# Optimization experiments

Measured on AMD Instinct MI355X. Metric: run time of the kernel, lower is better.

## Reference

```python
import jax, jax.numpy as jnp
import numpy as np

B, N, C, H = 8, 1024, 768, 12
D = C // H          # head_dim = 64
M = 2 * D           # rand_feat_dim = 128
SCALE = D ** -0.5
EPS = 1e-12         # F.normalize eps


def _feature_map(z, rand_matrix):
    # z: [B,H,N,D] already multiplied by sqrt(scale); proj: [H,D,M]
    logits = jnp.einsum('bhnd,hdm->bhnm', z, rand_matrix)
    sqnorm = 0.5 * jnp.sum(z * z, axis=-1, keepdims=True)
    return jnp.exp(logits - sqnorm) * (M ** -0.5)


def setup_inputs() -> dict:
    key = jax.random.key(0)
    k1, k2, k3, k4, k5 = jax.random.split(key, 5)
    x = jax.random.normal(k1, (B, N, C), dtype=jnp.float32)
    qkv_w = jax.random.normal(k2, (3 * C, C), dtype=jnp.float32) * 0.02
    proj_w = jax.random.normal(k3, (C, C), dtype=jnp.float32) * 0.02
    proj_b = jax.random.normal(k4, (C,), dtype=jnp.float32) * 0.02
    rand_matrix = jax.random.normal(k5, (H, D, M), dtype=jnp.float32)
    return {"x": x, "qkv_w": qkv_w, "proj_w": proj_w, "proj_b": proj_b,
            "rand_matrix": rand_matrix}


def reference(x, qkv_w, proj_w, proj_b, rand_matrix):
    b, n, c = x.shape
    # qkv projection (torch Linear, no bias): [B,N,3C] -> [3,B,H,N,D]
    qkv = (x @ qkv_w.T).reshape(b, n, 3, H, D).transpose(2, 0, 3, 1, 4)
    q, k, v = qkv[0], qkv[1], qkv[2]
    sq = SCALE ** 0.5
    qf = _feature_map(q * sq, rand_matrix)   # [B,H,N,M]
    kf = _feature_map(k * sq, rand_matrix)   # [B,H,N,M]
    attn = jnp.einsum('bhnm,bhkm->bhnk', qf, kf)          # explicit O(N^2)
    denom = jnp.maximum(jnp.sum(jnp.abs(attn), axis=-1, keepdims=True), EPS)
    attn = attn / denom                                   # L1 normalize
    out = jnp.einsum('bhnk,bhkd->bhnd', attn, v)          # [B,H,N,D]
    out = out.transpose(0, 2, 1, 3).reshape(b, n, c)
    return out @ proj_w.T + proj_b
```

## Files before the change

kernel.cpp:

```cpp
#include <hip/hip_runtime.h>
#include <hip/hip_bf16.h>

#define PB 8
#define PN 1024
#define PC 768
#define PH 12
#define PD 64
#define PM 128
#define SQ 0.35355339059327373f
#define MSCALE 0.08838834764831843f

typedef _Float16 f16;
typedef f16 f16x8 __attribute__((ext_vector_type(8)));
typedef f16 f16x4 __attribute__((ext_vector_type(4)));
typedef float f32x4 __attribute__((ext_vector_type(4)));

#define GLL(src, dst) __builtin_amdgcn_global_load_lds( \
    (const __attribute__((address_space(1))) void*)(src), \
    (__attribute__((address_space(3))) void*)(dst), 16, 0, 0)

__global__ __launch_bounds__(192) void conv_all(
        const float* __restrict__ x, const float* __restrict__ qkv_w,
        const float* __restrict__ proj_w, const float* __restrict__ rm,
        f16* __restrict__ Ax, f16* __restrict__ Bqk, f16* __restrict__ Bp,
        f16* __restrict__ Rt, float* __restrict__ kvf, float* __restrict__ sf)
{
    const int bid = blockIdx.x;
    const int t = threadIdx.x;
    if (bid < 11264) {
        const float* src; f16* dst; int r;
        if (bid < 8192)       { src = x;      dst = Ax;  r = bid; }
        else if (bid < 10496) { src = qkv_w;  dst = Bqk; r = bid - 8192; }
        else                  { src = proj_w; dst = Bp;  r = bid - 10496; }
        const int c = t * 4;
        float4 v = *(const float4*)&src[(size_t)r * PC + c];
        f16x4 hv;
        hv.x = (f16)v.x; hv.y = (f16)v.y; hv.z = (f16)v.z; hv.w = (f16)v.w;
        *(f16x4*)&dst[(size_t)r * PC + c] = hv;
    } else if (bid < 11276) {
        const int h = bid - 11264;
        for (int e = t; e < PD * PM; e += 192)
            Rt[(size_t)h * 8192 + e] = (f16)rm[(size_t)h * 8192 + (e & 63) * PM + (e >> 6)];
    } else if (bid < 12300) {
        float4 z = make_float4(0.f, 0.f, 0.f, 0.f);
        *(float4*)&kvf[(size_t)(bid - 11276) * 768 + t * 4] = z;
    } else {
        float4 z = make_float4(0.f, 0.f, 0.f, 0.f);
        *(float4*)&sf[(size_t)(bid - 12300) * 768 + t * 4] = z;
    }
}

__global__ __launch_bounds__(256) void gemm_qkv(
        const f16* __restrict__ A,
        const f16* __restrict__ Bm,
        f16* __restrict__ zq, f16* __restrict__ zk, f16* __restrict__ vh,
        float* __restrict__ sqq, float* __restrict__ sqk)
{
    __shared__ f16 As[128 * 64];
    __shared__ f16 Bs[128 * 64];
    const int t = threadIdx.x;
    const int wave = t >> 6, lane = t & 63;
    const int wm = wave >> 1, wn = wave & 1;
    const int bi = blockIdx.x * 128, bj = blockIdx.y * 128;

    f32x4 acc[4][4] = {};

    const int rowi = lane >> 3;
    const int cb = (lane & 7) ^ ((lane >> 4) & 3);
    const f16* ApE = A + (size_t)(bi + wave * 32 + rowi) * PC + cb * 8;
    const f16* ApO = A + (size_t)(bi + wave * 32 + rowi) * PC + (cb ^ 4) * 8;
    const f16* BpE = Bm + (size_t)(bj + wave * 32 + rowi) * PC + cb * 8;
    const f16* BpO = Bm + (size_t)(bj + wave * 32 + rowi) * PC + (cb ^ 4) * 8;
    f16* AsB = &As[wave * 32 * 64];
    f16* BsB = &Bs[wave * 32 * 64];

    const int q4 = lane >> 4;
    for (int kt = 0; kt < 12; ++kt) {
        const int k0 = kt * 64;
        __syncthreads();
        GLL(ApE + k0,               AsB);
        GLL(ApO + k0 + (size_t) 8 * PC, AsB + 8 * 64);
        GLL(ApE + k0 + (size_t)16 * PC, AsB + 16 * 64);
        GLL(ApO + k0 + (size_t)24 * PC, AsB + 24 * 64);
        GLL(BpE + k0,               BsB);
        GLL(BpO + k0 + (size_t) 8 * PC, BsB + 8 * 64);
        GLL(BpE + k0 + (size_t)16 * PC, BsB + 16 * 64);
        GLL(BpO + k0 + (size_t)24 * PC, BsB + 24 * 64);
        __syncthreads();

        #pragma unroll
        for (int kh = 0; kh < 2; ++kh) {
            f16x8 af[4], bf[4];
            #pragma unroll
            for (int i = 0; i < 4; ++i) {
                const int r = wm * 64 + i * 16 + (lane & 15);
                const int p = (kh * 4 + q4) ^ ((r >> 1) & 7);
                af[i] = *(const f16x8*)&As[r * 64 + p * 8];
            }
            #pragma unroll
            for (int j = 0; j < 4; ++j) {
                const int r = wn * 64 + j * 16 + (lane & 15);
                const int p = (kh * 4 + q4) ^ ((r >> 1) & 7);
                bf[j] = *(const f16x8*)&Bs[r * 64 + p * 8];
            }
            #pragma unroll
            for (int i = 0; i < 4; ++i)
                #pragma unroll
                for (int j = 0; j < 4; ++j)
                    acc[i][j] = __builtin_amdgcn_mfma_f32_16x16x32_f16(af[i], bf[j], acc[i][j], 0, 0, 0);
        }
    }

    const int quad = lane >> 4, cc = lane & 15;
    const int colbase = bj + wn * 64;
    const int b = bi >> 10;
    if (colbase < 1536) {
        const int which = colbase >= 768;
        const int h = (colbase - which * 768) >> 6;
        f16* zdst = which ? zk : zq;
        float* sdst = which ? sqk : sqq;
        const size_t bh = (size_t)(b * PH + h);
        #pragma unroll
        for (int i = 0; i < 4; ++i) {
            const int row0 = bi + wm * 64 + i * 16 + quad * 4;
            #pragma unroll
            for (int r = 0; r < 4; ++r) {
                const int n = (row0 + r) & 1023;
                f16 zh[4]; float psq = 0.f;
                #pragma unroll
                for (int j = 0; j < 4; ++j) {
                    zh[j] = (f16)(acc[i][j][r] * SQ);
                    float zf = (float)zh[j];
                    psq += zf * zf;
                }
                psq += __shfl_xor(psq, 1, 64);
                psq += __shfl_xor(psq, 2, 64);
                psq += __shfl_xor(psq, 4, 64);
                psq += __shfl_xor(psq, 8, 64);
                if (cc == 0) sdst[(bh << 10) + n] = 0.5f * psq;
                f16* zp = zdst + (((bh << 10) + n) << 6);
                #pragma unroll
                for (int j = 0; j < 4; ++j) zp[j * 16 + cc] = zh[j];
            }
        }
    } else {
        const int h = (colbase - 1536) >> 6;
        const size_t bh = (size_t)(b * PH + h);
        #pragma unroll
        for (int i = 0; i < 4; ++i) {
            const int row0 = bi + wm * 64 + i * 16 + quad * 4;
            #pragma unroll
            for (int r = 0; r < 4; ++r) {
                const int n = (row0 + r) & 1023;
                f16* vp = vh + (((bh << 10) + n) << 6);
                #pragma unroll
                for (int j = 0; j < 4; ++j) vp[j * 16 + cc] = (f16)acc[i][j][r];
            }
        }
    }
}

__global__ __launch_bounds__(256) void feat_kv(
        const f16* __restrict__ zk, const f16* __restrict__ Rt,
        const float* __restrict__ sqk, const f16* __restrict__ vh,
        float* __restrict__ kvf, float* __restrict__ sf)
{
    __shared__ __align__(16) char smem[52224];
    f16* As = (f16*)smem;
    f16* Bs = (f16*)(smem + 16384);
    f16* Pt = (f16*)smem;
    f16* vT = (f16*)(smem + 34816);
    __shared__ float sqs[128];

    const int t = threadIdx.x;
    const int wave = t >> 6, lane = t & 63;
    const int wm = wave >> 1, wn = wave & 1;
    const int nt = blockIdx.x, bh = blockIdx.y;
    const int h = bh % PH;

    const f16* A = zk + (((size_t)bh << 10) + nt * 128) * 64;
    const f16* Bm = Rt + (size_t)h * (PM * PD);

    if (t < 128) sqs[t] = sqk[((size_t)bh << 10) + nt * 128 + t];

    const int rowi = lane >> 3;
    const int cb = (lane & 7) ^ ((lane >> 4) & 3);
    const f16* ApE = A + (size_t)(wave * 32 + rowi) * 64 + cb * 8;
    const f16* ApO = A + (size_t)(wave * 32 + rowi) * 64 + (cb ^ 4) * 8;
    const f16* BpE = Bm + (size_t)(wave * 32 + rowi) * 64 + cb * 8;
    const f16* BpO = Bm + (size_t)(wave * 32 + rowi) * 64 + (cb ^ 4) * 8;
    f16* AsB = &As[wave * 32 * 64];
    f16* BsB = &Bs[wave * 32 * 64];
    GLL(ApE,            AsB);
    GLL(ApO + 8 * 64,   AsB + 8 * 64);
    GLL(ApE + 16 * 64,  AsB + 16 * 64);
    GLL(ApO + 24 * 64,  AsB + 24 * 64);
    GLL(BpE,            BsB);
    GLL(BpO + 8 * 64,   BsB + 8 * 64);
    GLL(BpE + 16 * 64,  BsB + 16 * 64);
    GLL(BpO + 24 * 64,  BsB + 24 * 64);
    __syncthreads();

    const int q4 = lane >> 4;
    f32x4 acc[4][4] = {};
    #pragma unroll
    for (int kh = 0; kh < 2; ++kh) {
        f16x8 af[4], bf[4];
        #pragma unroll
        for (int i = 0; i < 4; ++i) {
            const int r = wm * 64 + i * 16 + (lane & 15);
            const int p = (kh * 4 + q4) ^ ((r >> 1) & 7);
            af[i] = *(const f16x8*)&As[r * 64 + p * 8];
        }
        #pragma unroll
        for (int j = 0; j < 4; ++j) {
            const int r = wn * 64 + j * 16 + (lane & 15);
            const int p = (kh * 4 + q4) ^ ((r >> 1) & 7);
            bf[j] = *(const f16x8*)&Bs[r * 64 + p * 8];
        }
        #pragma unroll
        for (int i = 0; i < 4; ++i)
            #pragma unroll
            for (int j = 0; j < 4; ++j)
                acc[i][j] = __builtin_amdgcn_mfma_f32_16x16x32_f16(af[i], bf[j], acc[i][j], 0, 0, 0);
    }

    const int quad = lane >> 4, cc = lane & 15;
    __syncthreads();

    #pragma unroll
    for (int i = 0; i < 4; ++i) {
        #pragma unroll
        for (int j = 0; j < 4; ++j) {
            const int col = wn * 64 + j * 16 + cc;
            #pragma unroll
            for (int r = 0; r < 4; ++r) {
                const int rl = wm * 64 + i * 16 + quad * 4 + r;
                Pt[col * 136 + rl] = (f16)(__expf(acc[i][j][r] - sqs[rl]) * MSCALE);
            }
        }
    }
    {
        const int vn = t >> 1;
        const int vhf = (t & 1) * 32;
        const f16* vbase = vh + (((size_t)bh << 10) + nt * 128 + vn) * 64 + vhf;
        #pragma unroll
        for (int k = 0; k < 4; ++k) {
            f16x8 vv = *(const f16x8*)&vbase[k * 8];
            #pragma unroll
            for (int e = 0; e < 8; ++e)
                vT[(vhf + k * 8 + e) * 136 + vn] = vv[e];
        }
    }
    __syncthreads();

    f32x4 acc2[4][2] = {};
    #pragma unroll
    for (int kt = 0; kt < 4; ++kt) {
        const int kb = kt * 32 + (lane >> 4) * 8;
        f16x8 af2[4], bf2[2];
        #pragma unroll
        for (int i = 0; i < 4; ++i)
            af2[i] = *(const f16x8*)&Pt[(wm * 64 + i * 16 + (lane & 15)) * 136 + kb];
        #pragma unroll
        for (int j = 0; j < 2; ++j)
            bf2[j] = *(const f16x8*)&vT[(wn * 32 + j * 16 + (lane & 15)) * 136 + kb];
        #pragma unroll
        for (int i = 0; i < 4; ++i)
            #pragma unroll
            for (int j = 0; j < 2; ++j)
                acc2[i][j] = __builtin_amdgcn_mfma_f32_16x16x32_f16(af2[i], bf2[j], acc2[i][j], 0, 0, 0);
    }

    float* kvo = kvf + (size_t)bh * 8192;
    #pragma unroll
    for (int i = 0; i < 4; ++i) {
        #pragma unroll
        for (int j = 0; j < 2; ++j) {
            const int d = wn * 32 + j * 16 + cc;
            #pragma unroll
            for (int r = 0; r < 4; ++r) {
                const int m = wm * 64 + i * 16 + quad * 4 + r;
                atomicAdd(&kvo[m * 64 + d], acc2[i][j][r]);
            }
        }
    }
    {
        const int sm = t >> 1, shf = (t & 1) * 64;
        float sp = 0.f;
        #pragma unroll
        for (int k = 0; k < 8; ++k) {
            f16x8 pv = *(const f16x8*)&Pt[sm * 136 + shf + k * 8];
            #pragma unroll
            for (int e = 0; e < 8; ++e) sp += (float)pv[e];
        }
        sp += __shfl_xor(sp, 1, 64);
        if ((t & 1) == 0) atomicAdd(&sf[(size_t)bh * 128 + sm], sp);
    }
}

__global__ __launch_bounds__(256) void feat_apply(
        const f16* __restrict__ zq, const f16* __restrict__ Rt,
        const float* __restrict__ sqq, const float* __restrict__ kvf,
        const float* __restrict__ sf, f16* __restrict__ ohA)
{
    __shared__ __align__(16) char smem[52224];
    f16* As = (f16*)smem;
    f16* Bs = (f16*)(smem + 16384);
    f16* Pn = (f16*)smem;
    f16* kvT = (f16*)(smem + 34816);
    __shared__ float sqs[128], ssm[128], dns[128];

    const int t = threadIdx.x;
    const int wave = t >> 6, lane = t & 63;
    const int wm = wave >> 1, wn = wave & 1;
    const int nt = blockIdx.x, bh = blockIdx.y;
    const int b = bh / PH, h = bh % PH;

    const f16* A = zq + (((size_t)bh << 10) + nt * 128) * 64;
    const f16* Bm = Rt + (size_t)h * (PM * PD);

    if (t < 128) {
        sqs[t] = sqq[((size_t)bh << 10) + nt * 128 + t];
        ssm[t] = sf[(size_t)bh * 128 + t];
    }

    const int rowi = lane >> 3;
    const int cb = (lane & 7) ^ ((lane >> 4) & 3);
    const f16* ApE = A + (size_t)(wave * 32 + rowi) * 64 + cb * 8;
    const f16* ApO = A + (size_t)(wave * 32 + rowi) * 64 + (cb ^ 4) * 8;
    const f16* BpE = Bm + (size_t)(wave * 32 + rowi) * 64 + cb * 8;
    const f16* BpO = Bm + (size_t)(wave * 32 + rowi) * 64 + (cb ^ 4) * 8;
    f16* AsB = &As[wave * 32 * 64];
    f16* BsB = &Bs[wave * 32 * 64];
    GLL(ApE,            AsB);
    GLL(ApO + 8 * 64,   AsB + 8 * 64);
    GLL(ApE + 16 * 64,  AsB + 16 * 64);
    GLL(ApO + 24 * 64,  AsB + 24 * 64);
    GLL(BpE,            BsB);
    GLL(BpO + 8 * 64,   BsB + 8 * 64);
    GLL(BpE + 16 * 64,  BsB + 16 * 64);
    GLL(BpO + 24 * 64,  BsB + 24 * 64);
    __syncthreads();

    const int q4 = lane >> 4;
    f32x4 acc[4][4] = {};
    #pragma unroll
    for (int kh = 0; kh < 2; ++kh) {
        f16x8 af[4], bf[4];
        #pragma unroll
        for (int i = 0; i < 4; ++i) {
            const int r = wm * 64 + i * 16 + (lane & 15);
            const int p = (kh * 4 + q4) ^ ((r >> 1) & 7);
            af[i] = *(const f16x8*)&As[r * 64 + p * 8];
        }
        #pragma unroll
        for (int j = 0; j < 4; ++j) {
            const int r = wn * 64 + j * 16 + (lane & 15);
            const int p = (kh * 4 + q4) ^ ((r >> 1) & 7);
            bf[j] = *(const f16x8*)&Bs[r * 64 + p * 8];
        }
        #pragma unroll
        for (int i = 0; i < 4; ++i)
            #pragma unroll
            for (int j = 0; j < 4; ++j)
                acc[i][j] = __builtin_amdgcn_mfma_f32_16x16x32_f16(af[i], bf[j], acc[i][j], 0, 0, 0);
    }

    const int quad = lane >> 4, cc = lane & 15;
    __syncthreads();

    #pragma unroll
    for (int i = 0; i < 4; ++i) {
        #pragma unroll
        for (int j = 0; j < 4; ++j) {
            const int col = wn * 64 + j * 16 + cc;
            #pragma unroll
            for (int r = 0; r < 4; ++r) {
                const int rl = wm * 64 + i * 16 + quad * 4 + r;
                Pn[rl * 136 + col] = (f16)(__expf(acc[i][j][r] - sqs[rl]) * MSCALE);
            }
        }
    }
    {
        const int m = t >> 1;
        const int dh2 = (t & 1) * 32;
        const float* kvb = kvf + ((size_t)bh * 128 + m) * 64 + dh2;
        #pragma unroll
        for (int k = 0; k < 8; ++k) {
            float4 k4 = *(const float4*)&kvb[k * 4];
            kvT[(dh2 + k * 4 + 0) * 136 + m] = (f16)k4.x;
            kvT[(dh2 + k * 4 + 1) * 136 + m] = (f16)k4.y;
            kvT[(dh2 + k * 4 + 2) * 136 + m] = (f16)k4.z;
            kvT[(dh2 + k * 4 + 3) * 136 + m] = (f16)k4.w;
        }
    }
    __syncthreads();

    {
        const int n = t >> 1, mh = (t & 1) * 64;
        float p = 0.f;
        #pragma unroll
        for (int k = 0; k < 8; ++k) {
            f16x8 pv = *(const f16x8*)&Pn[n * 136 + mh + k * 8];
            #pragma unroll
            for (int e = 0; e < 8; ++e)
                p += (float)pv[e] * ssm[mh + k * 8 + e];
        }
        p += __shfl_xor(p, 1, 64);
        if ((t & 1) == 0) dns[n] = (p < 1e-12f) ? 1e-12f : p;
    }
    __syncthreads();

    f32x4 acc3[4][2] = {};
    #pragma unroll
    for (int kt = 0; kt < 4; ++kt) {
        const int kb = kt * 32 + (lane >> 4) * 8;
        f16x8 af3[4], bf3[2];
        #pragma unroll
        for (int i = 0; i < 4; ++i)
            af3[i] = *(const f16x8*)&Pn[(wm * 64 + i * 16 + (lane & 15)) * 136 + kb];
        #pragma unroll
        for (int j = 0; j < 2; ++j)
            bf3[j] = *(const f16x8*)&kvT[(wn * 32 + j * 16 + (lane & 15)) * 136 + kb];
        #pragma unroll
        for (int i = 0; i < 4; ++i)
            #pragma unroll
            for (int j = 0; j < 2; ++j)
                acc3[i][j] = __builtin_amdgcn_mfma_f32_16x16x32_f16(af3[i], bf3[j], acc3[i][j], 0, 0, 0);
    }

    f16* ob = ohA + ((size_t)(b * PN) + nt * 128) * PC + h * PD;
    #pragma unroll
    for (int i = 0; i < 4; ++i) {
        #pragma unroll
        for (int j = 0; j < 2; ++j) {
            const int d = wn * 32 + j * 16 + cc;
            #pragma unroll
            for (int r = 0; r < 4; ++r) {
                const int n = wm * 64 + i * 16 + quad * 4 + r;
                ob[(size_t)n * PC + d] = (f16)(acc3[i][j][r] / dns[n]);
            }
        }
    }
}

__global__ __launch_bounds__(256) void gemm_proj(
        const f16* __restrict__ A,
        const f16* __restrict__ Bm,
        float* __restrict__ Cm, const float* __restrict__ bias)
{
    __shared__ f16 As[128 * 64];
    __shared__ f16 Bs[64 * 64];
    const int t = threadIdx.x;
    const int wave = t >> 6, lane = t & 63;
    const int wm = wave >> 1, wn = wave & 1;
    const int bi = blockIdx.x * 128, bj = blockIdx.y * 64;

    f32x4 acc[4][2] = {};

    const int rowi = lane >> 3;
    const int cb = (lane & 7) ^ ((lane >> 4) & 3);
    const f16* ApE = A + (size_t)(bi + wave * 32 + rowi) * PC + cb * 8;
    const f16* ApO = A + (size_t)(bi + wave * 32 + rowi) * PC + (cb ^ 4) * 8;
    const f16* BpE = Bm + (size_t)(bj + wave * 16 + rowi) * PC + cb * 8;
    const f16* BpO = Bm + (size_t)(bj + wave * 16 + rowi) * PC + (cb ^ 4) * 8;
    f16* AsB = &As[wave * 32 * 64];
    f16* BsB = &Bs[wave * 16 * 64];

    const int q4 = lane >> 4;
    for (int kt = 0; kt < 12; ++kt) {
        const int k0 = kt * 64;
        __syncthreads();
        GLL(ApE + k0,               AsB);
        GLL(ApO + k0 + (size_t) 8 * PC, AsB + 8 * 64);
        GLL(ApE + k0 + (size_t)16 * PC, AsB + 16 * 64);
        GLL(ApO + k0 + (size_t)24 * PC, AsB + 24 * 64);
        GLL(BpE + k0,               BsB);
        GLL(BpO + k0 + (size_t) 8 * PC, BsB + 8 * 64);
        __syncthreads();

        #pragma unroll
        for (int kh = 0; kh < 2; ++kh) {
            f16x8 af[4], bf[2];
            #pragma unroll
            for (int i = 0; i < 4; ++i) {
                const int r = wm * 64 + i * 16 + (lane & 15);
                const int p = (kh * 4 + q4) ^ ((r >> 1) & 7);
                af[i] = *(const f16x8*)&As[r * 64 + p * 8];
            }
            #pragma unroll
            for (int j = 0; j < 2; ++j) {
                const int r = wn * 32 + j * 16 + (lane & 15);
                const int p = (kh * 4 + q4) ^ ((r >> 1) & 7);
                bf[j] = *(const f16x8*)&Bs[r * 64 + p * 8];
            }
            #pragma unroll
            for (int i = 0; i < 4; ++i)
                #pragma unroll
                for (int j = 0; j < 2; ++j)
                    acc[i][j] = __builtin_amdgcn_mfma_f32_16x16x32_f16(af[i], bf[j], acc[i][j], 0, 0, 0);
        }
    }

    const int cr = (lane >> 4) * 4, cc = lane & 15;
    #pragma unroll
    for (int i = 0; i < 4; ++i) {
        const int row = bi + wm * 64 + i * 16 + cr;
        #pragma unroll
        for (int j = 0; j < 2; ++j) {
            const int col = bj + wn * 32 + j * 16 + cc;
            const float bv = bias[col];
            #pragma unroll
            for (int r = 0; r < 4; ++r)
                Cm[(size_t)(row + r) * PC + col] = acc[i][j][r] + bv;
        }
    }
}

extern "C" void kernel_launch(void* const* d_in, const int* in_sizes, int n_in,
                              void* d_out, int out_size, void* d_ws, size_t ws_size,
                              hipStream_t stream) {
    const float* x      = (const float*)d_in[0];
    const float* qkv_w  = (const float*)d_in[1];
    const float* proj_w = (const float*)d_in[2];
    const float* proj_b = (const float*)d_in[3];
    const float* rm     = (const float*)d_in[4];
    float* out = (float*)d_out;

    char* ws = (char*)d_ws;
    f16*   Ax   = (f16*)(ws);
    f16*   Bqk  = (f16*)(ws + 12582912);
    f16*   Bp   = (f16*)(ws + 16121856);
    f16*   Rt   = (f16*)(ws + 17301504);
    f16*   zq   = (f16*)(ws + 17498112);
    f16*   zk   = (f16*)(ws + 30081024);
    f16*   vh   = (f16*)(ws + 42663936);
    float* sqq  = (float*)(ws + 55246848);
    float* sqk  = (float*)(ws + 55640064);
    float* kvf  = (float*)(ws + 56033280);
    float* sf   = (float*)(ws + 59179008);
    f16*   ohA  = (f16*)(ws + 59228160);

    conv_all<<<12316, 192, 0, stream>>>(x, qkv_w, proj_w, rm, Ax, Bqk, Bp, Rt, kvf, sf);

    gemm_qkv<<<dim3(64, 18), 256, 0, stream>>>(Ax, Bqk, zq, zk, vh, sqq, sqk);

    feat_kv<<<dim3(8, 96), 256, 0, stream>>>(zk, Rt, sqk, vh, kvf, sf);

    feat_apply<<<dim3(8, 96), 256, 0, stream>>>(zq, Rt, sqq, kvf, sf, ohA);

    gemm_proj<<<dim3(64, 12), 256, 0, stream>>>(ohA, Bp, out, proj_b);
}
```

Baseline: 191.1 us.

## Use 256x256 double-buffered 8-wave QKV GEMM and deterministic KV partial reduction

The QKV projection GEMM is rewritten to use 256x256 tiles with 512 threads, double-buffered LDS staging through global_load_lds, and an interleaved load/MFMA schedule with explicit barriers, waitcnts and setprio. The aim is more data reuse per tile and overlap of global loads with matrix math. Separately, feat_kv now writes per-tile partial KV and feature sums into scratch buffers instead of using atomics, and a new kv_reduce kernel sums them. This removes the zero-init and the atomic contention at the cost of an extra launch and extra memory traffic. The scratch buffers reuse workspace regions that are already dead at that point, such as Ax, Bqk and ohA.

```diff
diff --git a/kernel.cpp b/kernel.cpp
--- a/kernel.cpp
+++ b/kernel.cpp
@@ -19,11 +19,15 @@
     (const __attribute__((address_space(1))) void*)(src), \
     (__attribute__((address_space(3))) void*)(dst), 16, 0, 0)
 
+#define BARX() do { asm volatile("" ::: "memory"); __builtin_amdgcn_s_barrier(); asm volatile("" ::: "memory"); } while(0)
+#define LGKM0() asm volatile("s_waitcnt lgkmcnt(0)" ::: "memory")
+#define VMW(n)  asm volatile("s_waitcnt vmcnt(" #n ")" ::: "memory")
+
 __global__ __launch_bounds__(192) void conv_all(
         const float* __restrict__ x, const float* __restrict__ qkv_w,
         const float* __restrict__ proj_w, const float* __restrict__ rm,
         f16* __restrict__ Ax, f16* __restrict__ Bqk, f16* __restrict__ Bp,
-        f16* __restrict__ Rt, float* __restrict__ kvf, float* __restrict__ sf)
+        f16* __restrict__ Rt)
 {
     const int bid = blockIdx.x;
     const int t = threadIdx.x;
@@ -37,79 +41,116 @@
         f16x4 hv;
         hv.x = (f16)v.x; hv.y = (f16)v.y; hv.z = (f16)v.z; hv.w = (f16)v.w;
         *(f16x4*)&dst[(size_t)r * PC + c] = hv;
-    } else if (bid < 11276) {
+    } else {
         const int h = bid - 11264;
         for (int e = t; e < PD * PM; e += 192)
             Rt[(size_t)h * 8192 + e] = (f16)rm[(size_t)h * 8192 + (e & 63) * PM + (e >> 6)];
-    } else if (bid < 12300) {
-        float4 z = make_float4(0.f, 0.f, 0.f, 0.f);
-        *(float4*)&kvf[(size_t)(bid - 11276) * 768 + t * 4] = z;
-    } else {
-        float4 z = make_float4(0.f, 0.f, 0.f, 0.f);
-        *(float4*)&sf[(size_t)(bid - 12300) * 768 + t * 4] = z;
     }
 }
 
-__global__ __launch_bounds__(256) void gemm_qkv(
+__global__ __launch_bounds__(512) void gemm_qkv8(
         const f16* __restrict__ A,
         const f16* __restrict__ Bm,
         f16* __restrict__ zq, f16* __restrict__ zk, f16* __restrict__ vh,
         float* __restrict__ sqq, float* __restrict__ sqk)
 {
-    __shared__ f16 As[128 * 64];
-    __shared__ f16 Bs[128 * 64];
+    __shared__ f16 As[2][16384];
+    __shared__ f16 Bs[2][16384];
+
     const int t = threadIdx.x;
     const int wave = t >> 6, lane = t & 63;
-    const int wm = wave >> 1, wn = wave & 1;
-    const int bi = blockIdx.x * 128, bj = blockIdx.y * 128;
-
-    f32x4 acc[4][4] = {};
-
-    const int rowi = lane >> 3;
-    const int cb = (lane & 7) ^ ((lane >> 4) & 3);
-    const f16* ApE = A + (size_t)(bi + wave * 32 + rowi) * PC + cb * 8;
-    const f16* ApO = A + (size_t)(bi + wave * 32 + rowi) * PC + (cb ^ 4) * 8;
-    const f16* BpE = Bm + (size_t)(bj + wave * 32 + rowi) * PC + cb * 8;
-    const f16* BpO = Bm + (size_t)(bj + wave * 32 + rowi) * PC + (cb ^ 4) * 8;
-    f16* AsB = &As[wave * 32 * 64];
-    f16* BsB = &Bs[wave * 32 * 64];
-
-    const int q4 = lane >> 4;
-    for (int kt = 0; kt < 12; ++kt) {
-        const int k0 = kt * 64;
-        __syncthreads();
-        GLL(ApE + k0,               AsB);
-        GLL(ApO + k0 + (size_t) 8 * PC, AsB + 8 * 64);
-        GLL(ApE + k0 + (size_t)16 * PC, AsB + 16 * 64);
-        GLL(ApO + k0 + (size_t)24 * PC, AsB + 24 * 64);
-        GLL(BpE + k0,               BsB);
-        GLL(BpO + k0 + (size_t) 8 * PC, BsB + 8 * 64);
-        GLL(BpE + k0 + (size_t)16 * PC, BsB + 16 * 64);
-        GLL(BpO + k0 + (size_t)24 * PC, BsB + 24 * 64);
-        __syncthreads();
-
-        #pragma unroll
-        for (int kh = 0; kh < 2; ++kh) {
-            f16x8 af[4], bf[4];
-            #pragma unroll
-            for (int i = 0; i < 4; ++i) {
-                const int r = wm * 64 + i * 16 + (lane & 15);
-                const int p = (kh * 4 + q4) ^ ((r >> 1) & 7);
-                af[i] = *(const f16x8*)&As[r * 64 + p * 8];
-            }
-            #pragma unroll
-            for (int j = 0; j < 4; ++j) {
-                const int r = wn * 64 + j * 16 + (lane & 15);
-                const int p = (kh * 4 + q4) ^ ((r >> 1) & 7);
-                bf[j] = *(const f16x8*)&Bs[r * 64 + p * 8];
-            }
-            #pragma unroll
-            for (int i = 0; i < 4; ++i)
-                #pragma unroll
-                for (int j = 0; j < 4; ++j)
-                    acc[i][j] = __builtin_amdgcn_mfma_f32_16x16x32_f16(af[i], bf[j], acc[i][j], 0, 0, 0);
-        }
-    }
+    const int wm = wave >> 2, wn = wave & 3;
+    const int l15 = lane & 15, q4 = lane >> 4;
+    const int bi = blockIdx.x * 256, bj = blockIdx.y * 256;
+
+    const int srow = t >> 3;
+    const int schk = (t & 7) ^ ((t >> 4) & 7);
+    const f16* sA = A  + (size_t)(bi + srow) * PC + schk * 8;
+    const f16* sB = Bm + (size_t)(bj + srow) * PC + schk * 8;
+
+#define STAGE_A(BUF, H, KT) do { \
+    GLL(sA + (size_t)((H) * 128)      * PC + (KT) * 64, &As[BUF][(H) * 8192 +        wave * 512]); \
+    GLL(sA + (size_t)((H) * 128 + 64) * PC + (KT) * 64, &As[BUF][(H) * 8192 + 4096 + wave * 512]); } while(0)
+#define STAGE_B(BUF, H, KT) do { \
+    GLL(sB + (size_t)((H) * 128)      * PC + (KT) * 64, &Bs[BUF][(H) * 8192 +        wave * 512]); \
+    GLL(sB + (size_t)((H) * 128 + 64) * PC + (KT) * 64, &Bs[BUF][(H) * 8192 + 4096 + wave * 512]); } while(0)
+
+    f16x8 af[2][4], bfA[2][2], bfB[2][2];
+    f32x4 acc[8][4] = {};
+
+#define PH_LDA(BUF, RQ) \
+    _Pragma("unroll") for (int kh = 0; kh < 2; ++kh) \
+    _Pragma("unroll") for (int i = 0; i < 4; ++i) { \
+        const int row = wm * 128 + (RQ) * 64 + i * 16 + l15; \
+        const int p = (kh * 4 + q4) ^ ((row >> 1) & 7); \
+        af[kh][i] = *(const f16x8*)&As[BUF][row * 64 + p * 8]; }
+#define PH_LDB(BUF, CQ, BF) \
+    _Pragma("unroll") for (int kh = 0; kh < 2; ++kh) \
+    _Pragma("unroll") for (int j = 0; j < 2; ++j) { \
+        const int row = wn * 64 + (CQ) * 32 + j * 16 + l15; \
+        const int p = (kh * 4 + q4) ^ ((row >> 1) & 7); \
+        BF[kh][j] = *(const f16x8*)&Bs[BUF][row * 64 + p * 8]; }
+#define PH_MFMA(RQ, CQ, BF) \
+    _Pragma("unroll") for (int kh = 0; kh < 2; ++kh) \
+    _Pragma("unroll") for (int i = 0; i < 4; ++i) \
+    _Pragma("unroll") for (int j = 0; j < 2; ++j) \
+        acc[(RQ) * 4 + i][(CQ) * 2 + j] = __builtin_amdgcn_mfma_f32_16x16x32_f16( \
+            af[kh][i], BF[kh][j], acc[(RQ) * 4 + i][(CQ) * 2 + j], 0, 0, 0);
+
+    STAGE_A(0, 0, 0); STAGE_A(0, 1, 0); STAGE_B(0, 0, 0); STAGE_B(0, 1, 0);
+    STAGE_A(1, 0, 1);
+    VMW(2); BARX();
+
+    for (int u = 0; u < 12; u += 2) {
+        PH_LDA(0, 0);
+        PH_LDB(0, 0, bfA);
+        STAGE_A(1, 1, u + 1);
+        BARX(); LGKM0();
+        __builtin_amdgcn_s_setprio(1); PH_MFMA(0, 0, bfA); __builtin_amdgcn_s_setprio(0);
+        BARX();
+        PH_LDB(0, 1, bfB);
+        STAGE_B(1, 0, u + 1);
+        BARX(); LGKM0();
+        __builtin_amdgcn_s_setprio(1); PH_MFMA(0, 1, bfB); __builtin_amdgcn_s_setprio(0);
+        BARX();
+        PH_LDA(0, 1);
+        STAGE_B(1, 1, u + 1);
+        BARX(); LGKM0();
+        __builtin_amdgcn_s_setprio(1); PH_MFMA(1, 0, bfA); __builtin_amdgcn_s_setprio(0);
+        BARX();
+        if (u < 10) STAGE_A(0, 0, u + 2);
+        BARX(); LGKM0();
+        __builtin_amdgcn_s_setprio(1); PH_MFMA(1, 1, bfB); __builtin_amdgcn_s_setprio(0);
+        if (u < 10) { VMW(2); } else { VMW(0); }
+        BARX();
+        PH_LDA(1, 0);
+        PH_LDB(1, 0, bfA);
+        if (u < 10) STAGE_A(0, 1, u + 2);
+        BARX(); LGKM0();
+        __builtin_amdgcn_s_setprio(1); PH_MFMA(0, 0, bfA); __builtin_amdgcn_s_setprio(0);
+        BARX();
+        PH_LDB(1, 1, bfB);
+        if (u < 10) STAGE_B(0, 0, u + 2);
+        BARX(); LGKM0();
+        __builtin_amdgcn_s_setprio(1); PH_MFMA(0, 1, bfB); __builtin_amdgcn_s_setprio(0);
+        BARX();
+        PH_LDA(1, 1);
+        if (u < 10) STAGE_B(0, 1, u + 2);
+        BARX(); LGKM0();
+        __builtin_amdgcn_s_setprio(1); PH_MFMA(1, 0, bfA); __builtin_amdgcn_s_setprio(0);
+        BARX();
+        if (u < 9) STAGE_A(1, 0, u + 3);
+        BARX(); LGKM0();
+        __builtin_amdgcn_s_setprio(1); PH_MFMA(1, 1, bfB); __builtin_amdgcn_s_setprio(0);
+        if (u < 10) { VMW(2); }
+        BARX();
+    }
+
+#undef STAGE_A
+#undef STAGE_B
+#undef PH_LDA
+#undef PH_LDB
+#undef PH_MFMA
 
     const int quad = lane >> 4, cc = lane & 15;
     const int colbase = bj + wn * 64;
@@ -121,8 +162,8 @@
         float* sdst = which ? sqk : sqq;
         const size_t bh = (size_t)(b * PH + h);
         #pragma unroll
-        for (int i = 0; i < 4; ++i) {
-            const int row0 = bi + wm * 64 + i * 16 + quad * 4;
+        for (int i = 0; i < 8; ++i) {
+            const int row0 = bi + wm * 128 + i * 16 + quad * 4;
             #pragma unroll
             for (int r = 0; r < 4; ++r) {
                 const int n = (row0 + r) & 1023;
@@ -147,8 +188,8 @@
         const int h = (colbase - 1536) >> 6;
         const size_t bh = (size_t)(b * PH + h);
         #pragma unroll
-        for (int i = 0; i < 4; ++i) {
-            const int row0 = bi + wm * 64 + i * 16 + quad * 4;
+        for (int i = 0; i < 8; ++i) {
+            const int row0 = bi + wm * 128 + i * 16 + quad * 4;
             #pragma unroll
             for (int r = 0; r < 4; ++r) {
                 const int n = (row0 + r) & 1023;
@@ -163,7 +204,7 @@
 __global__ __launch_bounds__(256) void feat_kv(
         const f16* __restrict__ zk, const f16* __restrict__ Rt,
         const float* __restrict__ sqk, const f16* __restrict__ vh,
-        float* __restrict__ kvf, float* __restrict__ sf)
+        float* __restrict__ kvpA, float* __restrict__ kvpB, float* __restrict__ sfp)
 {
     __shared__ __align__(16) char smem[52224];
     f16* As = (f16*)smem;
@@ -272,7 +313,8 @@
                 acc2[i][j] = __builtin_amdgcn_mfma_f32_16x16x32_f16(af2[i], bf2[j], acc2[i][j], 0, 0, 0);
     }
 
-    float* kvo = kvf + (size_t)bh * 8192;
+    float* kvo = ((nt < 4) ? (kvpA + (size_t)nt * 786432)
+                           : (kvpB + (size_t)(nt - 4) * 786432)) + (size_t)bh * 8192;
     #pragma unroll
     for (int i = 0; i < 4; ++i) {
         #pragma unroll
@@ -281,7 +323,7 @@
             #pragma unroll
             for (int r = 0; r < 4; ++r) {
                 const int m = wm * 64 + i * 16 + quad * 4 + r;
-                atomicAdd(&kvo[m * 64 + d], acc2[i][j][r]);
+                kvo[m * 64 + d] = acc2[i][j][r];
             }
         }
     }
@@ -295,8 +337,39 @@
             for (int e = 0; e < 8; ++e) sp += (float)pv[e];
         }
         sp += __shfl_xor(sp, 1, 64);
-        if ((t & 1) == 0) atomicAdd(&sf[(size_t)bh * 128 + sm], sp);
-    }
+        if ((t & 1) == 0) sfp[((size_t)nt * 96 + bh) * 128 + sm] = sp;
+    }
+}
+
+__global__ __launch_bounds__(256) void kv_reduce(
+        const float* __restrict__ kvpA, const float* __restrict__ kvpB,
+        const float* __restrict__ sfp, float* __restrict__ kvf, float* __restrict__ sf)
+{
+    const int bh = blockIdx.x;
+    if (blockIdx.y == 8) {
+        const int t = threadIdx.x;
+        if (t < 128) {
+            float s = 0.f;
+            #pragma unroll
+            for (int nt = 0; nt < 8; ++nt)
+                s += sfp[((size_t)nt * 96 + bh) * 128 + t];
+            sf[(size_t)bh * 128 + t] = s;
+        }
+        return;
+    }
+    const size_t base = (size_t)bh * 8192 + blockIdx.y * 1024 + threadIdx.x * 4;
+    float4 s = *(const float4*)&kvpA[base];
+    #pragma unroll
+    for (int nt = 1; nt < 4; ++nt) {
+        float4 v = *(const float4*)&kvpA[(size_t)nt * 786432 + base];
+        s.x += v.x; s.y += v.y; s.z += v.z; s.w += v.w;
+    }
+    #pragma unroll
+    for (int nt = 0; nt < 4; ++nt) {
+        float4 v = *(const float4*)&kvpB[(size_t)nt * 786432 + base];
+        s.x += v.x; s.y += v.y; s.z += v.z; s.w += v.w;
+    }
+    *(float4*)&kvf[base] = s;
 }
 
 __global__ __launch_bounds__(256) void feat_apply(
@@ -542,11 +615,17 @@
     float* sf   = (float*)(ws + 59179008);
     f16*   ohA  = (f16*)(ws + 59228160);
 
-    conv_all<<<12316, 192, 0, stream>>>(x, qkv_w, proj_w, rm, Ax, Bqk, Bp, Rt, kvf, sf);
-
-    gemm_qkv<<<dim3(64, 18), 256, 0, stream>>>(Ax, Bqk, zq, zk, vh, sqq, sqk);
-
-    feat_kv<<<dim3(8, 96), 256, 0, stream>>>(zk, Rt, sqk, vh, kvf, sf);
+    float* kvpA = (float*)(ws);
+    float* kvpB = (float*)(ws + 59228160);
+    float* sfp  = (float*)(ws + 12582912);
+
+    conv_all<<<11276, 192, 0, stream>>>(x, qkv_w, proj_w, rm, Ax, Bqk, Bp, Rt);
+
+    gemm_qkv8<<<dim3(32, 9), 512, 0, stream>>>(Ax, Bqk, zq, zk, vh, sqq, sqk);
+
+    feat_kv<<<dim3(8, 96), 256, 0, stream>>>(zk, Rt, sqk, vh, kvpA, kvpB, sfp);
+
+    kv_reduce<<<dim3(96, 9), 256, 0, stream>>>(kvpA, kvpB, sfp, kvf, sf);
 
     feat_apply<<<dim3(8, 96), 256, 0, stream>>>(zq, Rt, sqq, kvf, sf, ohA);
 
```

Result: no change. 190.1 us (-0.5%).
